# Performance work log

Hardware: AMD Instinct MI355X
Metric: run time of the kernel (lower is better)

Reference implementation:

```python
import jax, jax.numpy as jnp
import numpy as np

EMBED_DIM = 768
N_HEADS = 12
HEAD_DIM = EMBED_DIM // N_HEADS
SCALE = HEAD_DIM ** 0.5


def setup_inputs() -> dict:
    key = jax.random.key(0)
    k1, k2, k3 = jax.random.split(key, 3)
    x = jax.random.normal(k1, (2, 2048, EMBED_DIM), dtype=jnp.float32)
    # weights stored [in, out] so forward is x @ W (equivalent to torch Linear with W.T)
    w_qkv = jax.random.normal(k2, (EMBED_DIM, 3 * EMBED_DIM), dtype=jnp.float32) * (EMBED_DIM ** -0.5)
    w_proj = jax.random.normal(k3, (EMBED_DIM, EMBED_DIM), dtype=jnp.float32) * (EMBED_DIM ** -0.5)
    return {"x": x, "w_qkv": w_qkv, "w_proj": w_proj}


def reference(x, w_qkv, w_proj):
    B, N, C = x.shape
    qkv = x @ w_qkv  # [B, N, 3C]
    qkv = qkv.reshape(B, N, 3, N_HEADS, HEAD_DIM)
    qkv = jnp.transpose(qkv, (2, 0, 3, 1, 4))  # [3, B, H, N, hd]
    q, k, v = qkv[0], qkv[1], qkv[2]
    attn = jnp.einsum("bhnd,bhmd->bhnm", q, k) / SCALE  # [B, H, N, N]
    attn = jax.nn.softmax(attn, axis=-1)
    out = jnp.einsum("bhnm,bhmd->bhnd", attn, v)  # [B, H, N, hd]
    out = jnp.transpose(out, (0, 2, 1, 3)).reshape(B, N, C)
    return out @ w_proj
```

## Files before the change

kernel.cpp:

```cpp
#include <hip/hip_runtime.h>
#include <hip/hip_bf16.h>
#include <stdint.h>

typedef uint16_t u16;
typedef __attribute__((ext_vector_type(4))) float f32x4;
typedef __attribute__((ext_vector_type(8))) short bf16x8;

#define LOG2E 1.4426950408889634f

static __device__ __forceinline__ u16 f2b(float x){
  union { float f; uint32_t u; } a; a.f = x;
  uint32_t r = a.u + 0x7FFFu + ((a.u >> 16) & 1u);
  return (u16)(r >> 16);
}

static __device__ __forceinline__ uint32_t pkrhu(float lo, float hi){
  union { float f; uint32_t u; } a, b; a.f = lo; b.f = hi;
  return __builtin_amdgcn_perm(b.u + 0x8000u, a.u + 0x8000u, 0x07060302u);
}

#define GLD16(g, l) __builtin_amdgcn_global_load_lds((const __attribute__((address_space(1))) void*)(g), (__attribute__((address_space(3))) void*)(l), 16, 0, 0)

__global__ __launch_bounds__(256) void k_prep(const float* __restrict__ x, u16* __restrict__ Xb,
                                              const float* __restrict__ wqkv, u16* __restrict__ WqkvT,
                                              const float* __restrict__ wproj, u16* __restrict__ WprojT){
  __shared__ float t[32][33];
  const int bid = blockIdx.x, tid = threadIdx.x;
  if (bid < 1536){
    int i = bid * 256 + tid;
    const f32x4* p = (const f32x4*)(x + (size_t)i * 8);
    f32x4 a = p[0], b = p[1];
    u16 h[8];
#pragma unroll
    for (int j = 0; j < 4; ++j){ h[j] = f2b(a[j]); h[4+j] = f2b(b[j]); }
    *(bf16x8*)(Xb + (size_t)i * 8) = *(const bf16x8*)h;
    return;
  }
  const float* in; u16* out; int R, C, bx, by;
  if (bid < 1536 + 1728){
    int q = bid - 1536; in = wqkv; out = WqkvT; R = 768; C = 2304; bx = q % 72; by = q / 72;
  } else {
    int q = bid - 1536 - 1728; in = wproj; out = WprojT; R = 768; C = 768; bx = q % 24; by = q / 24;
  }
  int c0 = bx * 32, r0 = by * 32;
  int tx = tid & 31, ty = tid >> 5;
#pragma unroll
  for (int i = 0; i < 32; i += 8) t[ty + i][tx] = in[(size_t)(r0 + ty + i) * C + c0 + tx];
  __syncthreads();
#pragma unroll
  for (int i = 0; i < 32; i += 8) out[(size_t)(c0 + ty + i) * R + r0 + tx] = f2b(t[tx][ty + i]);
}

__global__ __launch_bounds__(256) void k_gemmqkv(const u16* __restrict__ A, const u16* __restrict__ Bt,
                                                 u16* __restrict__ Qp, u16* __restrict__ Kp, u16* __restrict__ Vtp){
  __shared__ __align__(16) u16 SM[14336];
  u16* Al = SM; u16* Bl = SM + 8192;
  const int tid = threadIdx.x;
  const int w = tid >> 6, l = tid & 63;
  const int m0 = blockIdx.x * 128, n0 = blockIdx.y * 96;
  const int wm = (w >> 1) * 64, wn = (w & 1) * 48;
  const int lg = l >> 4, lr = l & 15;
  f32x4 acc[4][3] = {};
  const u16* asrc = A  + (size_t)(m0 + w*32 + (l >> 3)) * 768 + (l & 7) * 8;
  const u16* bsrc = Bt + (size_t)(n0 + w*24 + (l >> 3)) * 768 + (l & 7) * 8;
  for (int k0 = 0; k0 < 768; k0 += 64){
#pragma unroll
    for (int i = 0; i < 4; ++i)
      GLD16(asrc + (size_t)(i*8)*768 + k0, &Al[(w*32 + i*8) * 64]);
#pragma unroll
    for (int i = 0; i < 3; ++i)
      GLD16(bsrc + (size_t)(i*8)*768 + k0, &Bl[(w*24 + i*8) * 64]);
    __syncthreads();
    bf16x8 af[4][2], bfr[3][2];
#pragma unroll
    for (int mf = 0; mf < 4; ++mf)
#pragma unroll
      for (int ks = 0; ks < 2; ++ks)
        af[mf][ks] = *(const bf16x8*)&Al[(wm + mf*16 + lr) * 64 + ks*32 + lg*8];
#pragma unroll
    for (int nf = 0; nf < 3; ++nf)
#pragma unroll
      for (int ks = 0; ks < 2; ++ks)
        bfr[nf][ks] = *(const bf16x8*)&Bl[(wn + nf*16 + lr) * 64 + ks*32 + lg*8];
#pragma unroll
    for (int ks = 0; ks < 2; ++ks)
#pragma unroll
      for (int mf = 0; mf < 4; ++mf)
#pragma unroll
        for (int nf = 0; nf < 3; ++nf)
          acc[mf][nf] = __builtin_amdgcn_mfma_f32_16x16x32_bf16(af[mf][ks], bfr[nf][ks], acc[mf][nf], 0, 0, 0);
    __syncthreads();
  }

  const int which = n0 / 768;
  const int nl0 = n0 - which * 768;
  if (which < 2){
    u16* dst = (which == 0) ? Qp : Kp;
    const float sc = (which == 0) ? 0.125f * LOG2E : 1.0f;
#pragma unroll
    for (int mf = 0; mf < 4; ++mf)
#pragma unroll
      for (int nf = 0; nf < 3; ++nf)
#pragma unroll
        for (int r = 0; r < 4; ++r){
          int m = m0 + wm + mf*16 + lg*4 + r;
          int n = nl0 + wn + nf*16 + lr;
          int b = m >> 11, row = m & 2047, hh = n >> 6, d = n & 63;
          dst[(size_t)((b*12 + hh)*2048 + row) * 64 + d] = f2b(acc[mf][nf][r] * sc);
        }
  } else {
#pragma unroll
    for (int mf = 0; mf < 4; ++mf)
#pragma unroll
      for (int nf = 0; nf < 3; ++nf)
#pragma unroll
        for (int r = 0; r < 4; ++r){
          int mrow = wm + mf*16 + lg*4 + r;
          int c    = wn + nf*16 + lr;
          SM[c * 128 + mrow] = f2b(acc[mf][nf][r]);
        }
    __syncthreads();
#pragma unroll
    for (int rr = 0; rr < 6; ++rr){
      int c  = rr*16 + (tid >> 4);
      int mo = (tid & 15) * 8;
      bf16x8 v = *(const bf16x8*)&SM[c * 128 + mo];
      int n = nl0 + c, hh = n >> 6, d = n & 63;
      int m = m0 + mo, b = m >> 11, key = m & 2047;
      *(bf16x8*)&Vtp[(size_t)((b*12 + hh)*64 + d) * 2048 + key] = v;
    }
  }
}

__global__ __launch_bounds__(256) void k_gemm64(const u16* __restrict__ A, const u16* __restrict__ Bt,
                                                float* __restrict__ Co){
  __shared__ __align__(16) u16 SM[8192];
  u16* Al = SM; u16* Bl = SM + 4096;
  const int tid = threadIdx.x;
  const int w = tid >> 6, l = tid & 63;
  const int m0 = blockIdx.x * 64, n0 = blockIdx.y * 64;
  const int wm = (w >> 1) * 32, wn = (w & 1) * 32;
  const int lg = l >> 4, lr = l & 15;
  f32x4 acc[2][2] = {};
  const u16* asrc = A  + (size_t)(m0 + w*16 + (l >> 3)) * 768 + (l & 7) * 8;
  const u16* bsrc = Bt + (size_t)(n0 + w*16 + (l >> 3)) * 768 + (l & 7) * 8;
  for (int k0 = 0; k0 < 768; k0 += 64){
#pragma unroll
    for (int i = 0; i < 2; ++i){
      GLD16(asrc + (size_t)(i*8)*768 + k0, &Al[(w*16 + i*8) * 64]);
      GLD16(bsrc + (size_t)(i*8)*768 + k0, &Bl[(w*16 + i*8) * 64]);
    }
    __syncthreads();
    bf16x8 af[2][2], bfr[2][2];
#pragma unroll
    for (int mf = 0; mf < 2; ++mf)
#pragma unroll
      for (int ks = 0; ks < 2; ++ks){
        af[mf][ks]  = *(const bf16x8*)&Al[(wm + mf*16 + lr) * 64 + ks*32 + lg*8];
        bfr[mf][ks] = *(const bf16x8*)&Bl[(wn + mf*16 + lr) * 64 + ks*32 + lg*8];
      }
#pragma unroll
    for (int ks = 0; ks < 2; ++ks)
#pragma unroll
      for (int mf = 0; mf < 2; ++mf)
#pragma unroll
        for (int nf = 0; nf < 2; ++nf)
          acc[mf][nf] = __builtin_amdgcn_mfma_f32_16x16x32_bf16(af[mf][ks], bfr[nf][ks], acc[mf][nf], 0, 0, 0);
    __syncthreads();
  }
#pragma unroll
  for (int mf = 0; mf < 2; ++mf)
#pragma unroll
    for (int nf = 0; nf < 2; ++nf)
#pragma unroll
      for (int r = 0; r < 4; ++r)
        Co[(size_t)(m0 + wm + mf*16 + lg*4 + r) * 768 + n0 + wn + nf*16 + lr] = acc[mf][nf][r];
}

__global__ __launch_bounds__(512, 6) void k_attn(const u16* __restrict__ Qp, const u16* __restrict__ Kp,
                                                 const u16* __restrict__ Vtp, u16* __restrict__ AO){
  __shared__ __align__(16) u16 SM[24576];
  const int tid = threadIdx.x, w = tid >> 6, l = tid & 63;
  const int qh = w >> 2, kh = (w >> 1) & 1;
  const int QH = w >> 1, KH = w & 1;
  const int lg = l >> 4, lr = l & 15;
  const int qt_b = blockIdx.x, bh = blockIdx.y;
  const int b = bh / 12, hh = bh - b * 12;
  const size_t base = (size_t)bh * (2048 * 64);
  const u16* Qg = Qp + base; const u16* Kg = Kp + base; const u16* Vg = Vtp + base;
  const int q0w = qt_b * 64 + QH * 16;
  const int rsw = (lr & 7) * 8;

  bf16x8 qf[2];
#pragma unroll
  for (int ks = 0; ks < 2; ++ks)
    qf[ks] = *(const bf16x8*)&Qg[(size_t)(q0w + lr) * 64 + ks*32 + lg*8];

  f32x4 oacc[4] = {};
  float lp = 0.f;

  const int p_  = tid >> 3;
  const int sk  = 32*(p_ >> 5) + 8*((p_ >> 2) & 3) + 4*((p_ >> 4) & 1) + (p_ & 3);
  const int cs8 = (((tid & 7) ^ (p_ & 7)) << 3);
  const u16* kp = Kg + (size_t)sk * 64 + cs8;
  const u16* vp = Vg + ((size_t)p_ << 11) + cs8;
  const int drow = p_ * 64;
  u16* const K0 = SM + 0     + drow;  u16* const V0 = SM + 12288 + drow;
  u16* const K1 = SM + 4096  + drow;  u16* const V1 = SM + 16384 + drow;
  u16* const K2 = SM + 8192  + drow;  u16* const V2 = SM + 20480 + drow;

  auto compute = [&](const u16* Kc, const u16* Vc){
    f32x4 s[2] = {};
    bf16x8 kfr[2][2];
#pragma unroll
    for (int kf = 0; kf < 2; ++kf)
#pragma unroll
      for (int ks = 0; ks < 2; ++ks)
        kfr[kf][ks] = *(const bf16x8*)&Kc[(KH*32 + kf*16 + lr) * 64 + ((ks*32 + lg*8) ^ rsw)];
    __builtin_amdgcn_s_setprio(1);
#pragma unroll
    for (int ks = 0; ks < 2; ++ks)
#pragma unroll
      for (int kf = 0; kf < 2; ++kf)
        s[kf] = __builtin_amdgcn_mfma_f32_16x16x32_bf16(kfr[kf][ks], qf[ks], s[kf], 0, 0, 0);
    __builtin_amdgcn_s_setprio(0);

    float p00 = __builtin_exp2f(s[0][0]);
    float p01 = __builtin_exp2f(s[0][1]);
    float p02 = __builtin_exp2f(s[0][2]);
    float p03 = __builtin_exp2f(s[0][3]);
    float p10 = __builtin_exp2f(s[1][0]);
    float p11 = __builtin_exp2f(s[1][1]);
    float p12 = __builtin_exp2f(s[1][2]);
    float p13 = __builtin_exp2f(s[1][3]);
    lp += ((p00 + p01) + (p02 + p03)) + ((p10 + p11) + (p12 + p13));
    union { uint32_t u[4]; bf16x8 v; } fr;
    fr.u[0] = pkrhu(p00, p01);
    fr.u[1] = pkrhu(p02, p03);
    fr.u[2] = pkrhu(p10, p11);
    fr.u[3] = pkrhu(p12, p13);

    bf16x8 vfr[4];
#pragma unroll
    for (int nf = 0; nf < 4; ++nf)
      vfr[nf] = *(const bf16x8*)&Vc[(nf*16 + lr) * 64 + ((KH*32 + lg*8) ^ rsw)];
    __builtin_amdgcn_s_setprio(1);
#pragma unroll
    for (int nf = 0; nf < 4; ++nf)
      oacc[nf] = __builtin_amdgcn_mfma_f32_16x16x32_bf16(vfr[nf], fr.v, oacc[nf], 0, 0, 0);
    __builtin_amdgcn_s_setprio(0);
  };

#define STAGE2(KD, VD) do { GLD16(kp, KD); GLD16(vp, VD); kp += 4096; vp += 64; } while(0)
#define BAR_CNT2  do { asm volatile("s_waitcnt vmcnt(2)" ::: "memory"); \
                       __builtin_amdgcn_s_barrier(); __builtin_amdgcn_sched_barrier(0); } while(0)
#define BAR_CNT0  do { asm volatile("s_waitcnt vmcnt(0)" ::: "memory"); \
                       __builtin_amdgcn_s_barrier(); __builtin_amdgcn_sched_barrier(0); } while(0)

  STAGE2(K0, V0);
  STAGE2(K1, V1);
  BAR_CNT2;

  for (int g = 0; g < 10; ++g){
    STAGE2(K2, V2);  compute(SM + 0,    SM + 12288);  BAR_CNT2;
    STAGE2(K0, V0);  compute(SM + 4096, SM + 16384);  BAR_CNT2;
    STAGE2(K1, V1);  compute(SM + 8192, SM + 20480);  BAR_CNT2;
  }
  compute(SM + 0,    SM + 12288);
  BAR_CNT0;
  compute(SM + 4096, SM + 16384);

#undef STAGE2
#undef BAR_CNT2
#undef BAR_CNT0

  float lt = lp;
  lt += __shfl_xor(lt, 16);
  lt += __shfl_xor(lt, 32);

  __syncthreads();
  float* Osc = (float*)SM;
  float* Lsc = Osc + 64 * 65;
  if (KH == 1){
#pragma unroll
    for (int nf = 0; nf < 4; ++nf)
#pragma unroll
      for (int r = 0; r < 4; ++r)
        Osc[(QH*16 + lr) * 65 + nf*16 + lg*4 + r] = oacc[nf][r];
    if (lg == 0) Lsc[QH*16 + lr] = lt;
  }
  __syncthreads();
  if (KH == 0){
    float inv = 1.0f / (lt + Lsc[QH*16 + lr]);
#pragma unroll
    for (int nf = 0; nf < 4; ++nf)
#pragma unroll
      for (int r = 0; r < 4; ++r){
        float o = oacc[nf][r] + Osc[(QH*16 + lr) * 65 + nf*16 + lg*4 + r];
        AO[(size_t)((b << 11) + q0w + lr) * 768 + hh*64 + nf*16 + lg*4 + r] = f2b(o * inv);
      }
  }
}

extern "C" void kernel_launch(void* const* d_in, const int* in_sizes, int n_in,
                              void* d_out, int out_size, void* d_ws, size_t ws_size,
                              hipStream_t stream){
  const float* x      = (const float*)d_in[0];
  const float* w_qkv  = (const float*)d_in[1];
  const float* w_proj = (const float*)d_in[2];
  float* out = (float*)d_out;
  char* ws = (char*)d_ws;
  u16* Xb     = (u16*)(ws + 0);
  u16* WqkvT  = (u16*)(ws + 6291456);
  u16* WprojT = (u16*)(ws + 9830400);
  u16* Qp     = (u16*)(ws + 11010048);
  u16* Kp     = (u16*)(ws + 17301504);
  u16* Vtp    = (u16*)(ws + 23592960);
  u16* AO     = (u16*)(ws + 29884416);

  k_prep<<<3840, 256, 0, stream>>>(x, Xb, w_qkv, WqkvT, w_proj, WprojT);
  k_gemmqkv<<<dim3(32, 24), 256, 0, stream>>>(Xb, WqkvT, Qp, Kp, Vtp);
  k_attn<<<dim3(32, 24), 512, 0, stream>>>(Qp, Kp, Vtp, AO);
  k_gemm64<<<dim3(64, 12), 256, 0, stream>>>(AO, WprojT, out);
}
```

Before: 88.46 us.

## Load V fragments directly from global to registers and remap blocks for locality

The attention kernel stops staging V tiles through LDS and instead has each lane load its V MFMA fragments straight from global memory into registers every iteration. This halves the shared-memory footprint, which could raise occupancy, and removes the LDS write/read round trip for V. The grid is flattened and blocks are remapped so that consecutive blocks spread across XCDs, keeping all blocks of one head on the same XCD and its L2. The cost is that the direct V loads are issued just before use with little prefetch distance, so global-load latency may stall the PV MFMAs. The loads also use a strided access pattern.

```diff
diff --git a/kernel.cpp b/kernel.cpp
--- a/kernel.cpp
+++ b/kernel.cpp
@@ -179,12 +179,13 @@
 
 __global__ __launch_bounds__(512, 6) void k_attn(const u16* __restrict__ Qp, const u16* __restrict__ Kp,
                                                  const u16* __restrict__ Vtp, u16* __restrict__ AO){
-  __shared__ __align__(16) u16 SM[24576];
+  __shared__ __align__(16) u16 SM[12288];
   const int tid = threadIdx.x, w = tid >> 6, l = tid & 63;
-  const int qh = w >> 2, kh = (w >> 1) & 1;
   const int QH = w >> 1, KH = w & 1;
   const int lg = l >> 4, lr = l & 15;
-  const int qt_b = blockIdx.x, bh = blockIdx.y;
+  const int p = blockIdx.x;
+  const int lgid = ((p & 7) * 96) + (p >> 3);
+  const int qt_b = lgid & 31, bh = lgid >> 5;
   const int b = bh / 12, hh = bh - b * 12;
   const size_t base = (size_t)bh * (2048 * 64);
   const u16* Qg = Qp + base; const u16* Kg = Kp + base; const u16* Vg = Vtp + base;
@@ -203,13 +204,14 @@
   const int sk  = 32*(p_ >> 5) + 8*((p_ >> 2) & 3) + 4*((p_ >> 4) & 1) + (p_ & 3);
   const int cs8 = (((tid & 7) ^ (p_ & 7)) << 3);
   const u16* kp = Kg + (size_t)sk * 64 + cs8;
-  const u16* vp = Vg + ((size_t)p_ << 11) + cs8;
   const int drow = p_ * 64;
-  u16* const K0 = SM + 0     + drow;  u16* const V0 = SM + 12288 + drow;
-  u16* const K1 = SM + 4096  + drow;  u16* const V1 = SM + 16384 + drow;
-  u16* const K2 = SM + 8192  + drow;  u16* const V2 = SM + 20480 + drow;
-
-  auto compute = [&](const u16* Kc, const u16* Vc){
+  u16* const K0 = SM + 0    + drow;
+  u16* const K1 = SM + 4096 + drow;
+  u16* const K2 = SM + 8192 + drow;
+
+  const u16* vp = Vg + (size_t)lr * 2048 + KH*32 + lg*8;
+
+  auto compute = [&](const u16* Kc, const bf16x8* vfr){
     f32x4 s[2] = {};
     bf16x8 kfr[2][2];
 #pragma unroll
@@ -240,10 +242,6 @@
     fr.u[2] = pkrhu(p10, p11);
     fr.u[3] = pkrhu(p12, p13);
 
-    bf16x8 vfr[4];
-#pragma unroll
-    for (int nf = 0; nf < 4; ++nf)
-      vfr[nf] = *(const bf16x8*)&Vc[(nf*16 + lr) * 64 + ((KH*32 + lg*8) ^ rsw)];
     __builtin_amdgcn_s_setprio(1);
 #pragma unroll
     for (int nf = 0; nf < 4; ++nf)
@@ -251,27 +249,32 @@
     __builtin_amdgcn_s_setprio(0);
   };
 
-#define STAGE2(KD, VD) do { GLD16(kp, KD); GLD16(vp, VD); kp += 4096; vp += 64; } while(0)
-#define BAR_CNT2  do { asm volatile("s_waitcnt vmcnt(2)" ::: "memory"); \
+#define VLOAD(VF) do { _Pragma("unroll") \
+    for (int nf = 0; nf < 4; ++nf) VF[nf] = *(const bf16x8*)(vp + (size_t)nf * 32768); \
+    vp += 64; } while(0)
+#define STAGE1(KD) do { GLD16(kp, KD); kp += 4096; } while(0)
+#define BAR_CNT1  do { asm volatile("s_waitcnt vmcnt(1)" ::: "memory"); \
                        __builtin_amdgcn_s_barrier(); __builtin_amdgcn_sched_barrier(0); } while(0)
 #define BAR_CNT0  do { asm volatile("s_waitcnt vmcnt(0)" ::: "memory"); \
                        __builtin_amdgcn_s_barrier(); __builtin_amdgcn_sched_barrier(0); } while(0)
 
-  STAGE2(K0, V0);
-  STAGE2(K1, V1);
-  BAR_CNT2;
-
+  STAGE1(K0);
+  STAGE1(K1);
+  BAR_CNT1;
+
+  bf16x8 vfr[4];
   for (int g = 0; g < 10; ++g){
-    STAGE2(K2, V2);  compute(SM + 0,    SM + 12288);  BAR_CNT2;
-    STAGE2(K0, V0);  compute(SM + 4096, SM + 16384);  BAR_CNT2;
-    STAGE2(K1, V1);  compute(SM + 8192, SM + 20480);  BAR_CNT2;
-  }
-  compute(SM + 0,    SM + 12288);
+    VLOAD(vfr); STAGE1(K2); compute(SM + 0,    vfr); BAR_CNT1;
+    VLOAD(vfr); STAGE1(K0); compute(SM + 4096, vfr); BAR_CNT1;
+    VLOAD(vfr); STAGE1(K1); compute(SM + 8192, vfr); BAR_CNT1;
+  }
+  VLOAD(vfr); compute(SM + 0,    vfr);
   BAR_CNT0;
-  compute(SM + 4096, SM + 16384);
-
-#undef STAGE2
-#undef BAR_CNT2
+  VLOAD(vfr); compute(SM + 4096, vfr);
+
+#undef VLOAD
+#undef STAGE1
+#undef BAR_CNT1
 #undef BAR_CNT0
 
   float lt = lp;
@@ -320,6 +323,6 @@
 
   k_prep<<<3840, 256, 0, stream>>>(x, Xb, w_qkv, WqkvT, w_proj, WprojT);
   k_gemmqkv<<<dim3(32, 24), 256, 0, stream>>>(Xb, WqkvT, Qp, Kp, Vtp);
-  k_attn<<<dim3(32, 24), 512, 0, stream>>>(Qp, Kp, Vtp, AO);
+  k_attn<<<768, 512, 0, stream>>>(Qp, Kp, Vtp, AO);
   k_gemm64<<<dim3(64, 12), 256, 0, stream>>>(AO, WprojT, out);
 }
```

New measurement: 212.6 us. 2.4x slower.
